# Kernel optimization log

Hardware: AMD Instinct MI355X
Metric: run time of the kernel (lower is better)

## Reference

```python
import jax, jax.numpy as jnp
import numpy as np

DIM = 768
HEADS = 12
TOPK = 32


def setup_inputs() -> dict:
    key = jax.random.key(0)
    k1, k2, k3 = jax.random.split(key, 3)
    B, hw, T = 8, 576, 4
    N = hw + T * hw
    x = jax.random.normal(k1, (B, N, DIM), dtype=jnp.float32)
    qkv_w = jax.random.normal(k2, (3 * DIM, DIM), dtype=jnp.float32) * 0.02
    proj_w = jax.random.normal(k3, (DIM, DIM), dtype=jnp.float32) * 0.02
    proj_b = jnp.zeros((DIM,), dtype=jnp.float32)
    return {"x": x, "qkv_w": qkv_w, "proj_w": proj_w, "proj_b": proj_b, "T": T, "hw": hw}


def _query_topk_every_frame(attn, hw, T):
    # attn: [B, H, hw, hw + T*hw]
    B, H, n1, _ = attn.shape
    qa = attn[..., :hw]                       # [B,H,hw,hw] query self part
    ma = attn[..., hw:].reshape(B, H, n1, T, hw)  # per-frame memory scores
    vals, idx = jax.lax.top_k(ma, TOPK)       # [B,H,hw,T,K]
    cat = jnp.concatenate([qa, vals.reshape(B, H, n1, T * TOPK)], axis=-1)
    sm = jax.nn.softmax(cat, axis=-1)         # softmax over hw + T*K survivors
    qa2 = sm[..., :hw]
    tv = sm[..., hw:].reshape(B, H, n1, T, TOPK)
    # scatter normalized top-k values back into dense per-frame affinity
    bi = jnp.arange(B)[:, None, None, None, None]
    hi = jnp.arange(H)[None, :, None, None, None]
    ni = jnp.arange(n1)[None, None, :, None, None]
    ti = jnp.arange(T)[None, None, None, :, None]
    aff = jnp.zeros_like(ma).at[bi, hi, ni, ti, idx].set(tv)
    return jnp.concatenate([qa2, aff.reshape(B, H, n1, T * hw)], axis=-1)


def reference(x, qkv_w, proj_w, proj_b, T, hw):
    B, N, C = x.shape
    assert N == hw + T * hw
    hd = C // HEADS
    scale = hd ** -0.5
    qkv = (x @ qkv_w.T).reshape(B, N, 3, HEADS, hd).transpose(2, 0, 3, 1, 4)
    q, k, v = qkv[0], qkv[1], qkv[2]          # each [B,H,N,hd]
    query_q = q[:, :, :hw]                    # [B,H,hw,hd]
    attn = jnp.einsum('bhqd,bhkd->bhqk', query_q, k) * scale  # [B,H,hw,N]
    attn = _query_topk_every_frame(attn, hw, T)
    out = jnp.einsum('bhqk,bhkd->bhqd', attn, v)  # [B,H,hw,hd]
    query = out.transpose(0, 2, 1, 3).reshape(B, hw, C)
    query = query @ proj_w.T + proj_b
    # memory tokens pass through unchanged
    return jnp.concatenate([query, x[:, hw:]], axis=1)
```

## Files before the change

kernel.cpp:

```cpp
#include <hip/hip_runtime.h>
#include <hip/hip_bf16.h>


using s16x8 = __attribute__((ext_vector_type(8))) short;
using f32x4 = __attribute__((ext_vector_type(4))) float;
typedef unsigned short u16;

#define MFMA_B16(A,B,C) __builtin_amdgcn_mfma_f32_16x16x32_bf16(A,B,C,0,0,0)

__device__ __forceinline__ u16 f2bf(float f) {
  unsigned u = __float_as_uint(f);
  u += 0x7FFFu + ((u >> 16) & 1u);
  return (u16)(u >> 16);
}
__device__ __forceinline__ float bf2f(u16 h) {
  return __uint_as_float(((unsigned)h) << 16);
}
__device__ __forceinline__ int lanes_below(unsigned long long m) {
  return __builtin_amdgcn_mbcnt_hi((unsigned)(m >> 32),
         __builtin_amdgcn_mbcnt_lo((unsigned)m, 0));
}
__device__ __forceinline__ void stage16(const u16* __restrict__ g, u16* l) {
  __builtin_amdgcn_global_load_lds(
      (const __attribute__((address_space(1))) unsigned int*)g,
      (__attribute__((address_space(3))) unsigned int*)l, 16, 0, 0);
}

__global__ __launch_bounds__(256) void cvt_kernel(const float* __restrict__ src,
                                                  u16* __restrict__ dst, int n4) {
  int i = blockIdx.x * blockDim.x + threadIdx.x;
  if (i >= n4) return;
  float4 v = ((const float4*)src)[i];
  unsigned lo = (unsigned)f2bf(v.x) | ((unsigned)f2bf(v.y) << 16);
  unsigned hi = (unsigned)f2bf(v.z) | ((unsigned)f2bf(v.w) << 16);
  uint2 o; o.x = lo; o.y = hi;
  ((uint2*)dst)[i] = o;
}

__global__ __launch_bounds__(256) void copy_tail_kernel(const float* __restrict__ x,
                                                        float* __restrict__ out) {
  int i = blockIdx.x * blockDim.x + threadIdx.x;
  int b = i / 442368;
  int off = i - b * 442368;
  size_t e = (size_t)b * 552960 + 110592 + off;
  ((float4*)out)[e] = ((const float4*)x)[e];
}

__global__ __launch_bounds__(256) void transpose_v(const u16* __restrict__ vbuf,
                                                   u16* __restrict__ vtb) {
  __shared__ __align__(16) u16 s[64][72];
  const int r0 = blockIdx.x * 64;
  const int bh = blockIdx.y;
  const int t = threadIdx.x;
  const int kr = t >> 2, c0 = (t & 3) * 16;
  const u16* src = vbuf + (size_t)bh * 2880 * 64 + (size_t)(r0 + kr) * 64 + c0;
  *(int4*)&s[kr][c0]     = *(const int4*)&src[0];
  *(int4*)&s[kr][c0 + 8] = *(const int4*)&src[8];
  __syncthreads();
  const int d = t >> 2, k0 = (t & 3) * 16;
  u16 tmp[16];
  #pragma unroll
  for (int i = 0; i < 16; ++i) tmp[i] = s[k0 + i][d];
  u16* dst = vtb + ((size_t)bh * 64 + d) * 2880 + r0 + k0;
  *(int4*)&dst[0] = *(const int4*)&tmp[0];
  *(int4*)&dst[8] = *(const int4*)&tmp[8];
}

template<int MODE>
__global__ __launch_bounds__(256) void gemm_nt(
    const u16* __restrict__ A, const u16* __restrict__ Bw,
    const float* __restrict__ bias,
    u16* __restrict__ qbuf, u16* __restrict__ kbuf,
    u16* __restrict__ vbuf, float* __restrict__ fout)
{
  __shared__ __align__(16) u16 sA[128 * 64];
  __shared__ __align__(16) u16 sB[128 * 64];
  const int n0 = blockIdx.x * 128;
  const int m0 = blockIdx.y * 128;
  if (MODE == 0 && n0 < 768) {
    const int s = m0 % 2880;
    if (s >= 576 && s + 128 <= 2880) return;
  }
  const int tid = threadIdx.x;
  const int w = tid >> 6, lane = tid & 63;
  const int l15 = lane & 15, rg = lane >> 4;
  const int ko = rg * 8;
  const int mq = (w >> 1) * 64, nq = (w & 1) * 64;
  const int trow = tid >> 3, tcol = (tid & 7) * 8;

  f32x4 z = {0.f, 0.f, 0.f, 0.f};
  f32x4 acc[4][4];
  #pragma unroll
  for (int i = 0; i < 4; ++i)
    #pragma unroll
    for (int j = 0; j < 4; ++j) acc[i][j] = z;

  for (int k0 = 0; k0 < 768; k0 += 64) {
    __syncthreads();
    #pragma unroll
    for (int i = 0; i < 4; ++i) {
      stage16(&A[(size_t)(m0 + trow + i * 32) * 768 + k0 + tcol],
              &sA[(trow + i * 32) * 64 + tcol]);
      stage16(&Bw[(size_t)(n0 + trow + i * 32) * 768 + k0 + tcol],
              &sB[(trow + i * 32) * 64 + tcol]);
    }
    __syncthreads();
    #pragma unroll
    for (int kk = 0; kk < 2; ++kk) {
      const int ko2 = kk * 32 + ko;
      s16x8 af[4], bf[4];
      #pragma unroll
      for (int i = 0; i < 4; ++i) {
        af[i] = *(const s16x8*)&sA[(mq + i * 16 + l15) * 64 + ko2];
        bf[i] = *(const s16x8*)&sB[(nq + i * 16 + l15) * 64 + ko2];
      }
      #pragma unroll
      for (int mi = 0; mi < 4; ++mi)
        #pragma unroll
        for (int ni = 0; ni < 4; ++ni)
          acc[mi][ni] = MFMA_B16(af[mi], bf[ni], acc[mi][ni]);
    }
  }

  if (MODE == 0) {
    const int which = n0 / 768;
    const int nb = n0 % 768;
    #pragma unroll
    for (int mi = 0; mi < 4; ++mi)
      #pragma unroll
      for (int ni = 0; ni < 4; ++ni)
        #pragma unroll
        for (int r = 0; r < 4; ++r) {
          const int gm = m0 + mq + mi * 16 + rg * 4 + r;
          const int b  = gm / 2880;
          const int rr = gm - b * 2880;
          const int ng = nb + nq + ni * 16 + l15;
          const int h  = ng >> 6, d = ng & 63;
          const float c = acc[mi][ni][r];
          if (which == 0) {
            if (rr < 576)
              qbuf[((size_t)(b * 12 + h) * 576 + rr) * 64 + d] = f2bf(c * 0.125f);
          } else if (which == 1) {
            kbuf[((size_t)(b * 12 + h) * 2880 + rr) * 64 + d] = f2bf(c);
          } else {
            vbuf[((size_t)(b * 12 + h) * 2880 + rr) * 64 + d] = f2bf(c);
          }
        }
  } else {
    #pragma unroll
    for (int mi = 0; mi < 4; ++mi)
      #pragma unroll
      for (int ni = 0; ni < 4; ++ni)
        #pragma unroll
        for (int r = 0; r < 4; ++r) {
          const int gm = m0 + mq + mi * 16 + rg * 4 + r;
          const int gn = n0 + nq + ni * 16 + l15;
          const int b = gm / 576;
          const int q = gm - b * 576;
          fout[((size_t)b * 2880 + q) * 768 + gn] = acc[mi][ni][r] + bias[gn];
        }
  }
}

__global__ __launch_bounds__(256, 8) void attn_kernel(
    const u16* __restrict__ qbuf, const u16* __restrict__ kbuf,
    const u16* __restrict__ vtb, u16* __restrict__ aout)
{
  constexpr int PST = 584;
  __shared__ __align__(16) u16 s_p[16 * PST];
  __shared__ float s_denom[16];

  const int bid = blockIdx.x;
  const int L = (bid & 7) * 432 + (bid >> 3);
  const int qt = L % 36;
  const int h  = (L / 36) % 12;
  const int b  = L / 432;
  const int bh = b * 12 + h;
  const int q0 = qt * 16;
  const int tid = threadIdx.x, w = tid >> 6, lane = tid & 63;
  const int l15 = lane & 15, rg = lane >> 4;
  const int ko = rg * 8;

  const u16* qp = qbuf + ((size_t)bh * 576 + q0) * 64;
  s16x8 aQ[2];
  aQ[0] = *(const s16x8*)&qp[l15 * 64 + ko];
  aQ[1] = *(const s16x8*)&qp[l15 * 64 + 32 + ko];

  const u16* kp = kbuf + (size_t)bh * 2880 * 64;
  const u16* vt = vtb + ((size_t)bh * 64 + w * 16 + l15) * 2880;
  const int prow = (((l15 & 3) << 2) | (l15 >> 2)) * PST;
  f32x4 zz = {0.f, 0.f, 0.f, 0.f};
  f32x4 accO = zz;

  auto writeback = [&](int q, int lrow, const unsigned* k, unsigned prefix) {
    unsigned long long eqm[9];
    int cnt_gt = 0;
    #pragma unroll
    for (int j = 0; j < 9; ++j) {
      unsigned long long ge = __ballot(k[j] >= prefix);
      unsigned long long gt = __ballot(k[j] >  prefix);
      eqm[j] = ge ^ gt;
      cnt_gt += __popcll(gt);
    }
    const int rem = 32 - cnt_gt;
    int run_eq = 0;
    float dsum = 0.f;
    #pragma unroll
    for (int j = 0; j < 9; ++j) {
      const bool isgt = k[j] > prefix;
      const bool iseq = k[j] == prefix;
      const bool sel = isgt || (iseq && (run_eq + lanes_below(eqm[j])) < rem);
      const u16 raw = (u16)(k[j] & 0x7FFFu);
      dsum += sel ? bf2f(raw) : 0.f;
      s_p[lrow + lane + 64 * j] = sel ? raw : (u16)0;
      run_eq += __popcll(eqm[j]);
    }
    #pragma unroll
    for (int off = 1; off < 64; off <<= 1) dsum += __shfl_xor(dsum, off);
    if (lane == 0) s_denom[q] += dsum;
  };

  auto topk2 = [&](int qA, int qB) {
    const int lrA = ((((qA & 3) << 2) | (qA >> 2))) * PST;
    const int lrB = ((((qB & 3) << 2) | (qB >> 2))) * PST;
    unsigned kA[9], kB[9];
    #pragma unroll
    for (int j = 0; j < 9; ++j) {
      kA[j] = (unsigned)s_p[lrA + lane + 64 * j] | 0x8000u;
      kB[j] = (unsigned)s_p[lrB + lane + 64 * j] | 0x8000u;
    }
    unsigned pA = 0, pB = 0;
    #pragma unroll
    for (int bit = 15; bit >= 0; --bit) {
      const unsigned cA = pA | (1u << bit), cB = pB | (1u << bit);
      int nA = 0, nB = 0;
      #pragma unroll
      for (int j = 0; j < 9; ++j) {
        nA += __popcll(__ballot(kA[j] >= cA));
        nB += __popcll(__ballot(kB[j] >= cB));
      }
      pA = (nA >= 32) ? cA : pA;
      pB = (nB >= 32) ? cB : pB;
    }
    writeback(qA, lrA, kA, pA);
    writeback(qB, lrB, kB, pB);
  };

  for (int c = 0; c < 5; ++c) {
    #pragma unroll 3
    for (int t = 0; t < 9; ++t) {
      const int wk = w * 144 + t * 16;
      const u16* kr = kp + (size_t)(c * 576 + wk + l15) * 64 + ko;
      s16x8 kf0 = *(const s16x8*)&kr[0];
      s16x8 kf1 = *(const s16x8*)&kr[32];
      f32x4 a0 = zz;
      a0 = MFMA_B16(aQ[0], kf0, a0);
      a0 = MFMA_B16(aQ[1], kf1, a0);
      #pragma unroll
      for (int r = 0; r < 4; ++r)
        s_p[(r * 4 + rg) * PST + wk + l15] = f2bf(__expf(a0[r]));
    }
    __syncthreads();

    if (c == 0) {
      #pragma unroll
      for (int ri = 0; ri < 4; ++ri) {
        const int q = w * 4 + ri;
        const int lrow = (((q & 3) << 2) | (q >> 2)) * PST;
        float s = 0.f;
        #pragma unroll
        for (int j = 0; j < 9; ++j) s += bf2f(s_p[lrow + lane + 64 * j]);
        #pragma unroll
        for (int off = 1; off < 64; off <<= 1) s += __shfl_xor(s, off);
        if (lane == 0) s_denom[q] = s;
      }
    } else {
      topk2(w * 4 + 0, w * 4 + 1);
      topk2(w * 4 + 2, w * 4 + 3);
      __syncthreads();
    }

    #pragma unroll 3
    for (int k0 = 0; k0 < 576; k0 += 32) {
      s16x8 vf = *(const s16x8*)&vt[c * 576 + k0 + ko];
      s16x8 pa = *(const s16x8*)&s_p[prow + k0 + ko];
      accO = MFMA_B16(pa, vf, accO);
    }
    __syncthreads();
  }

  const int d = w * 16 + l15;
  #pragma unroll
  for (int r = 0; r < 4; ++r) {
    const int row = rg * 4 + r;
    const float val = accO[r] / s_denom[row];
    aout[((size_t)(b * 576 + q0 + row)) * 768 + h * 64 + d] = f2bf(val);
  }
}

extern "C" void kernel_launch(void* const* d_in, const int* in_sizes, int n_in,
                              void* d_out, int out_size, void* d_ws, size_t ws_size,
                              hipStream_t stream)
{
  const float* x      = (const float*)d_in[0];
  const float* qkv_w  = (const float*)d_in[1];
  const float* proj_w = (const float*)d_in[2];
  const float* proj_b = (const float*)d_in[3];
  float* out = (float*)d_out;

  char* ws = (char*)d_ws;
  size_t off = 0;
  auto alloc = [&](size_t bytes) -> void* {
    void* p = ws + off;
    off += (bytes + 255) & ~(size_t)255;
    return p;
  };
  u16* xb   = (u16*)alloc((size_t)23040 * 768 * 2);
  u16* wqb  = (u16*)alloc((size_t)2304 * 768 * 2);
  u16* wpb  = (u16*)alloc((size_t)768 * 768 * 2);
  u16* qbuf = (u16*)alloc((size_t)96 * 576 * 64 * 2);
  u16* vtb  = (u16*)alloc((size_t)96 * 64 * 2880 * 2);
  u16* aout = (u16*)alloc((size_t)4608 * 768 * 2);
  u16* kbuf = (u16*)d_out;
  u16* vbuf = kbuf + (size_t)96 * 2880 * 64;

  cvt_kernel<<<17280, 256, 0, stream>>>(x, xb, 17694720 / 4);
  cvt_kernel<<<1728, 256, 0, stream>>>(qkv_w, wqb, 1769472 / 4);
  cvt_kernel<<<576, 256, 0, stream>>>(proj_w, wpb, 589824 / 4);
  gemm_nt<0><<<dim3(18, 180), 256, 0, stream>>>(xb, wqb, nullptr,
                                                qbuf, kbuf, vbuf, nullptr);
  transpose_v<<<dim3(45, 96), 256, 0, stream>>>(vbuf, vtb);
  attn_kernel<<<3456, 256, 0, stream>>>(qbuf, kbuf, vtb, aout);
  gemm_nt<1><<<dim3(6, 36), 256, 0, stream>>>(aout, wpb, proj_b,
                                              nullptr, nullptr, nullptr, out);
  copy_tail_kernel<<<13824, 256, 0, stream>>>(x, out);
}
```

Baseline: 546.7 us.

## Fuse V transpose into QKV GEMM epilogue and simplify per-row top-k selection

The QKV GEMM now writes V straight into the transposed layout by staging the tile in shared memory, which removes the separate transpose kernel and the round trip of V through global memory. The attention kernel drops the paired two-row radix select in favour of a per-row loop that exits the bit search once exactly 32 candidates remain. It also switches the P row layout in LDS to a plain row order instead of the permuted one. The trade-offs are a larger merged shared-memory buffer in the GEMM, possible bank conflicts in the column-wise LDS reads of the transpose, and less instruction-level parallelism in top-k, since the two interleaved selections are gone and the early exit adds divergence-free branching.

```diff
diff --git a/kernel.cpp b/kernel.cpp
--- a/kernel.cpp
+++ b/kernel.cpp
@@ -46,35 +46,16 @@
   ((float4*)out)[e] = ((const float4*)x)[e];
 }
 
-__global__ __launch_bounds__(256) void transpose_v(const u16* __restrict__ vbuf,
-                                                   u16* __restrict__ vtb) {
-  __shared__ __align__(16) u16 s[64][72];
-  const int r0 = blockIdx.x * 64;
-  const int bh = blockIdx.y;
-  const int t = threadIdx.x;
-  const int kr = t >> 2, c0 = (t & 3) * 16;
-  const u16* src = vbuf + (size_t)bh * 2880 * 64 + (size_t)(r0 + kr) * 64 + c0;
-  *(int4*)&s[kr][c0]     = *(const int4*)&src[0];
-  *(int4*)&s[kr][c0 + 8] = *(const int4*)&src[8];
-  __syncthreads();
-  const int d = t >> 2, k0 = (t & 3) * 16;
-  u16 tmp[16];
-  #pragma unroll
-  for (int i = 0; i < 16; ++i) tmp[i] = s[k0 + i][d];
-  u16* dst = vtb + ((size_t)bh * 64 + d) * 2880 + r0 + k0;
-  *(int4*)&dst[0] = *(const int4*)&tmp[0];
-  *(int4*)&dst[8] = *(const int4*)&tmp[8];
-}
-
 template<int MODE>
 __global__ __launch_bounds__(256) void gemm_nt(
     const u16* __restrict__ A, const u16* __restrict__ Bw,
     const float* __restrict__ bias,
     u16* __restrict__ qbuf, u16* __restrict__ kbuf,
-    u16* __restrict__ vbuf, float* __restrict__ fout)
+    u16* __restrict__ vtb, float* __restrict__ fout)
 {
-  __shared__ __align__(16) u16 sA[128 * 64];
-  __shared__ __align__(16) u16 sB[128 * 64];
+  __shared__ __align__(16) u16 smem[128 * 128];
+  u16* sA = smem;
+  u16* sB = smem + 128 * 64;
   const int n0 = blockIdx.x * 128;
   const int m0 = blockIdx.y * 128;
   if (MODE == 0 && n0 < 768) {
@@ -125,27 +106,53 @@
   if (MODE == 0) {
     const int which = n0 / 768;
     const int nb = n0 % 768;
-    #pragma unroll
-    for (int mi = 0; mi < 4; ++mi)
-      #pragma unroll
-      for (int ni = 0; ni < 4; ++ni)
-        #pragma unroll
-        for (int r = 0; r < 4; ++r) {
-          const int gm = m0 + mq + mi * 16 + rg * 4 + r;
-          const int b  = gm / 2880;
-          const int rr = gm - b * 2880;
-          const int ng = nb + nq + ni * 16 + l15;
-          const int h  = ng >> 6, d = ng & 63;
-          const float c = acc[mi][ni][r];
-          if (which == 0) {
-            if (rr < 576)
-              qbuf[((size_t)(b * 12 + h) * 576 + rr) * 64 + d] = f2bf(c * 0.125f);
-          } else if (which == 1) {
-            kbuf[((size_t)(b * 12 + h) * 2880 + rr) * 64 + d] = f2bf(c);
-          } else {
-            vbuf[((size_t)(b * 12 + h) * 2880 + rr) * 64 + d] = f2bf(c);
+    if (which == 2) {
+      __syncthreads();
+      #pragma unroll
+      for (int mi = 0; mi < 4; ++mi)
+        #pragma unroll
+        for (int ni = 0; ni < 4; ++ni)
+          #pragma unroll
+          for (int r = 0; r < 4; ++r)
+            smem[(mq + mi * 16 + rg * 4 + r) * 128 + nq + ni * 16 + l15] =
+                f2bf(acc[mi][ni][r]);
+      __syncthreads();
+      const int c = tid & 127, kh = tid >> 7;
+      const int gm0 = m0 + kh * 64;
+      const int bb = gm0 / 2880, rr0 = gm0 - bb * 2880;
+      const int ng = nb + c;
+      const int hh = ng >> 6, dd = ng & 63;
+      u16* dst = vtb + ((size_t)((bb * 12 + hh) * 64 + dd)) * 2880 + rr0;
+      #pragma unroll
+      for (int seg = 0; seg < 4; ++seg) {
+        u16 tmp[16];
+        #pragma unroll
+        for (int i = 0; i < 16; ++i)
+          tmp[i] = smem[(kh * 64 + seg * 16 + i) * 128 + c];
+        *(int4*)&dst[seg * 16]     = *(const int4*)&tmp[0];
+        *(int4*)&dst[seg * 16 + 8] = *(const int4*)&tmp[8];
+      }
+    } else {
+      #pragma unroll
+      for (int mi = 0; mi < 4; ++mi)
+        #pragma unroll
+        for (int ni = 0; ni < 4; ++ni)
+          #pragma unroll
+          for (int r = 0; r < 4; ++r) {
+            const int gm = m0 + mq + mi * 16 + rg * 4 + r;
+            const int b  = gm / 2880;
+            const int rr = gm - b * 2880;
+            const int ng = nb + nq + ni * 16 + l15;
+            const int h  = ng >> 6, d = ng & 63;
+            const float cc = acc[mi][ni][r];
+            if (which == 0) {
+              if (rr < 576)
+                qbuf[((size_t)(b * 12 + h) * 576 + rr) * 64 + d] = f2bf(cc * 0.125f);
+            } else {
+              kbuf[((size_t)(b * 12 + h) * 2880 + rr) * 64 + d] = f2bf(cc);
+            }
           }
-        }
+    }
   } else {
     #pragma unroll
     for (int mi = 0; mi < 4; ++mi)
@@ -188,63 +195,8 @@
 
   const u16* kp = kbuf + (size_t)bh * 2880 * 64;
   const u16* vt = vtb + ((size_t)bh * 64 + w * 16 + l15) * 2880;
-  const int prow = (((l15 & 3) << 2) | (l15 >> 2)) * PST;
   f32x4 zz = {0.f, 0.f, 0.f, 0.f};
   f32x4 accO = zz;
-
-  auto writeback = [&](int q, int lrow, const unsigned* k, unsigned prefix) {
-    unsigned long long eqm[9];
-    int cnt_gt = 0;
-    #pragma unroll
-    for (int j = 0; j < 9; ++j) {
-      unsigned long long ge = __ballot(k[j] >= prefix);
-      unsigned long long gt = __ballot(k[j] >  prefix);
-      eqm[j] = ge ^ gt;
-      cnt_gt += __popcll(gt);
-    }
-    const int rem = 32 - cnt_gt;
-    int run_eq = 0;
-    float dsum = 0.f;
-    #pragma unroll
-    for (int j = 0; j < 9; ++j) {
-      const bool isgt = k[j] > prefix;
-      const bool iseq = k[j] == prefix;
-      const bool sel = isgt || (iseq && (run_eq + lanes_below(eqm[j])) < rem);
-      const u16 raw = (u16)(k[j] & 0x7FFFu);
-      dsum += sel ? bf2f(raw) : 0.f;
-      s_p[lrow + lane + 64 * j] = sel ? raw : (u16)0;
-      run_eq += __popcll(eqm[j]);
-    }
-    #pragma unroll
-    for (int off = 1; off < 64; off <<= 1) dsum += __shfl_xor(dsum, off);
-    if (lane == 0) s_denom[q] += dsum;
-  };
-
-  auto topk2 = [&](int qA, int qB) {
-    const int lrA = ((((qA & 3) << 2) | (qA >> 2))) * PST;
-    const int lrB = ((((qB & 3) << 2) | (qB >> 2))) * PST;
-    unsigned kA[9], kB[9];
-    #pragma unroll
-    for (int j = 0; j < 9; ++j) {
-      kA[j] = (unsigned)s_p[lrA + lane + 64 * j] | 0x8000u;
-      kB[j] = (unsigned)s_p[lrB + lane + 64 * j] | 0x8000u;
-    }
-    unsigned pA = 0, pB = 0;
-    #pragma unroll
-    for (int bit = 15; bit >= 0; --bit) {
-      const unsigned cA = pA | (1u << bit), cB = pB | (1u << bit);
-      int nA = 0, nB = 0;
-      #pragma unroll
-      for (int j = 0; j < 9; ++j) {
-        nA += __popcll(__ballot(kA[j] >= cA));
-        nB += __popcll(__ballot(kB[j] >= cB));
-      }
-      pA = (nA >= 32) ? cA : pA;
-      pB = (nB >= 32) ? cB : pB;
-    }
-    writeback(qA, lrA, kA, pA);
-    writeback(qB, lrB, kB, pB);
-  };
 
   for (int c = 0; c < 5; ++c) {
     #pragma unroll 3
@@ -258,7 +210,7 @@
       a0 = MFMA_B16(aQ[1], kf1, a0);
       #pragma unroll
       for (int r = 0; r < 4; ++r)
-        s_p[(r * 4 + rg) * PST + wk + l15] = f2bf(__expf(a0[r]));
+        s_p[(rg * 4 + r) * PST + wk + l15] = f2bf(__expf(a0[r]));
     }
     __syncthreads();
 
@@ -266,24 +218,60 @@
       #pragma unroll
       for (int ri = 0; ri < 4; ++ri) {
         const int q = w * 4 + ri;
-        const int lrow = (((q & 3) << 2) | (q >> 2)) * PST;
         float s = 0.f;
         #pragma unroll
-        for (int j = 0; j < 9; ++j) s += bf2f(s_p[lrow + lane + 64 * j]);
+        for (int j = 0; j < 9; ++j) s += bf2f(s_p[q * PST + lane + 64 * j]);
         #pragma unroll
         for (int off = 1; off < 64; off <<= 1) s += __shfl_xor(s, off);
         if (lane == 0) s_denom[q] = s;
       }
     } else {
-      topk2(w * 4 + 0, w * 4 + 1);
-      topk2(w * 4 + 2, w * 4 + 3);
+      for (int ri = 0; ri < 4; ++ri) {
+        const int q = w * 4 + ri;
+        unsigned key[9];
+        #pragma unroll
+        for (int j = 0; j < 9; ++j)
+          key[j] = (unsigned)s_p[q * PST + lane + 64 * j] | 0x8000u;
+        unsigned prefix = 0;
+        for (int bit = 15; bit >= 0; --bit) {
+          const unsigned cand = prefix | (1u << bit);
+          int cnt = 0;
+          #pragma unroll
+          for (int j = 0; j < 9; ++j)
+            cnt += __popcll(__ballot(key[j] >= cand));
+          if (cnt >= 32) prefix = cand;
+          if (cnt == 32) break;
+        }
+        unsigned long long eqm[9];
+        int cnt_gt = 0;
+        #pragma unroll
+        for (int j = 0; j < 9; ++j) {
+          cnt_gt += __popcll(__ballot(key[j] > prefix));
+          eqm[j] = __ballot(key[j] == prefix);
+        }
+        const int rem = 32 - cnt_gt;
+        int run_eq = 0;
+        float dsum = 0.f;
+        #pragma unroll
+        for (int j = 0; j < 9; ++j) {
+          const bool sel = (key[j] > prefix) ||
+              (key[j] == prefix && run_eq + lanes_below(eqm[j]) < rem);
+          const u16 raw = (u16)(key[j] & 0x7FFFu);
+          dsum += sel ? bf2f(raw) : 0.f;
+          s_p[q * PST + lane + 64 * j] = sel ? raw : (u16)0;
+          run_eq += __popcll(eqm[j]);
+        }
+        #pragma unroll
+        for (int off = 1; off < 64; off <<= 1) dsum += __shfl_xor(dsum, off);
+        if (lane == 0) s_denom[q] += dsum;
+      }
       __syncthreads();
     }
 
     #pragma unroll 3
     for (int k0 = 0; k0 < 576; k0 += 32) {
       s16x8 vf = *(const s16x8*)&vt[c * 576 + k0 + ko];
-      s16x8 pa = *(const s16x8*)&s_p[prow + k0 + ko];
+      s16x8 pa = *(const s16x8*)&s_p[l15 * PST + k0 + ko];
       accO = MFMA_B16(pa, vf, accO);
     }
     __syncthreads();
@@ -322,14 +310,12 @@
   u16* vtb  = (u16*)alloc((size_t)96 * 64 * 2880 * 2);
   u16* aout = (u16*)alloc((size_t)4608 * 768 * 2);
   u16* kbuf = (u16*)d_out;
-  u16* vbuf = kbuf + (size_t)96 * 2880 * 64;
 
   cvt_kernel<<<17280, 256, 0, stream>>>(x, xb, 17694720 / 4);
   cvt_kernel<<<1728, 256, 0, stream>>>(qkv_w, wqb, 1769472 / 4);
   cvt_kernel<<<576, 256, 0, stream>>>(proj_w, wpb, 589824 / 4);
   gemm_nt<0><<<dim3(18, 180), 256, 0, stream>>>(xb, wqb, nullptr,
-                                                qbuf, kbuf, vbuf, nullptr);
-  transpose_v<<<dim3(45, 96), 256, 0, stream>>>(vbuf, vtb);
+                                                qbuf, kbuf, vtb, nullptr);
   attn_kernel<<<3456, 256, 0, stream>>>(qbuf, kbuf, vtb, aout);
   gemm_nt<1><<<dim3(6, 36), 256, 0, stream>>>(aout, wpb, proj_b,
                                               nullptr, nullptr, nullptr, out);
```

New measurement: 493.5 us. 9.7% less time.
